# Optimization experiments

Hardware: AMD Instinct MI355X
Metric: run time of the kernel (lower is better)

The kernel has to match this reference:

```python
import jax, jax.numpy as jnp
import numpy as np

IN_FEATURES = 256
OUT_FEATURES = 128
ALPHA = 0.2  # LeakyReLU negative slope
NEG_INF = -9e15
N_NODES = 8192


def _xavier_uniform(key, shape, gain):
    fan_in, fan_out = shape[0], shape[1]
    limit = gain * np.sqrt(6.0 / (fan_in + fan_out))
    return jax.random.uniform(key, shape, jnp.float32, -limit, limit)


def setup_inputs() -> dict:
    key = jax.random.key(0)
    k_h, k_adj, k_W, k_a = jax.random.split(key, 4)
    h = jax.random.normal(k_h, (N_NODES, IN_FEATURES), dtype=jnp.float32)
    adj = jax.random.randint(k_adj, (N_NODES, N_NODES), 0, 2, dtype=jnp.int32)
    W = _xavier_uniform(k_W, (IN_FEATURES, OUT_FEATURES), gain=1.414)
    a = _xavier_uniform(k_a, (2 * OUT_FEATURES, 1), gain=1.414)
    return {"h": h, "adj": adj, "W": W, "a": a}


def reference(h, adj, W, a):
    # Wh: (N, F_out)
    Wh = h @ W
    # Decompose a = [a1; a2]; e_ij = leakyrelu(Wh_i . a1 + Wh_j . a2)
    # == the original concat([Wh_i, Wh_j]) @ a, without the O(N^2*2F) tensor.
    a1 = a[:OUT_FEATURES, 0]  # (F_out,)
    a2 = a[OUT_FEATURES:, 0]  # (F_out,)
    src = Wh @ a1  # (N,)
    dst = Wh @ a2  # (N,)
    e = jax.nn.leaky_relu(src[:, None] + dst[None, :], negative_slope=ALPHA)  # (N, N)
    attention = jnp.where(adj > 0, e, NEG_INF)
    attention = jax.nn.softmax(attention, axis=1)
    # dropout p=0.0 (eval) -> identity
    h_prime = attention @ Wh  # (N, F_out)
    return jax.nn.elu(h_prime)  # concat=True
```

## Files before the change

kernel.cpp:

```cpp
#include <hip/hip_runtime.h>

#define N_NODES 8192
#define IN_F    256
#define OUT_F   128
#define ALPHA_S 0.2f

typedef __attribute__((ext_vector_type(8))) short  short8;
typedef __attribute__((ext_vector_type(4))) short  short4v;
typedef __attribute__((ext_vector_type(4))) float  floatx4;
typedef __attribute__((ext_vector_type(4))) int    intx4;
typedef __attribute__((ext_vector_type(4))) float  fx4;

static __device__ __forceinline__ short f2bf(float f) {
    union { float f; unsigned int i; } u; u.f = f;
    unsigned int r = u.i + 0x7FFFu + ((u.i >> 16) & 1u);
    return (short)(r >> 16);
}

__global__ __launch_bounds__(512) void k_wh(
    const float* __restrict__ h,
    const float* __restrict__ W,
    const float* __restrict__ a,
    short* __restrict__ WhT,
    float* __restrict__ src,
    float* __restrict__ dst)
{
    __shared__ short Wt[OUT_F][IN_F + 8];
    __shared__ short htile[32][IN_F + 8];
    __shared__ float q1s[IN_F], q2s[IN_F];
    __shared__ short wh_t[OUT_F][40];

    const int t      = threadIdx.x;
    const int lane   = t & 63;
    const int wave   = t >> 6;
    const int r_base = blockIdx.x * 32;

#pragma unroll
    for (int rep = 0; rep < 4; ++rep) {
        const int idx = rep * 8192 + t * 16;
        const int k   = idx >> 7;
        const int f   = idx & 127;
        fx4 w0 = *(const fx4*)(W + idx);
        fx4 w1 = *(const fx4*)(W + idx + 4);
        fx4 w2 = *(const fx4*)(W + idx + 8);
        fx4 w3 = *(const fx4*)(W + idx + 12);
        fx4 a10 = *(const fx4*)(a + f);
        fx4 a11 = *(const fx4*)(a + f + 4);
        fx4 a12 = *(const fx4*)(a + f + 8);
        fx4 a13 = *(const fx4*)(a + f + 12);
        fx4 a20 = *(const fx4*)(a + OUT_F + f);
        fx4 a21 = *(const fx4*)(a + OUT_F + f + 4);
        fx4 a22 = *(const fx4*)(a + OUT_F + f + 8);
        fx4 a23 = *(const fx4*)(a + OUT_F + f + 12);
        float p1 = 0.f, p2 = 0.f;
#pragma unroll
        for (int e = 0; e < 4; ++e) {
            p1 = fmaf(w0[e], a10[e], p1); p2 = fmaf(w0[e], a20[e], p2);
            p1 = fmaf(w1[e], a11[e], p1); p2 = fmaf(w1[e], a21[e], p2);
            p1 = fmaf(w2[e], a12[e], p1); p2 = fmaf(w2[e], a22[e], p2);
            p1 = fmaf(w3[e], a13[e], p1); p2 = fmaf(w3[e], a23[e], p2);
        }
#pragma unroll
        for (int e = 0; e < 4; ++e) {
            Wt[f + e][k]      = f2bf(w0[e]);
            Wt[f + 4 + e][k]  = f2bf(w1[e]);
            Wt[f + 8 + e][k]  = f2bf(w2[e]);
            Wt[f + 12 + e][k] = f2bf(w3[e]);
        }
#pragma unroll
        for (int m = 1; m < 8; m <<= 1) {
            p1 += __shfl_xor(p1, m, 64);
            p2 += __shfl_xor(p2, m, 64);
        }
        if ((t & 7) == 0) { q1s[k] = p1; q2s[k] = p2; }
    }

    const int r0   = t >> 4;
    const int fgrp = t & 15;
    const int k0   = fgrp * 16;
    fx4 h0, h1, h2, h3;
    {
        const float* hp = h + (size_t)(r_base + r0) * IN_F + k0;
        h0 = *(const fx4*)hp; h1 = *(const fx4*)(hp + 4);
        h2 = *(const fx4*)(hp + 8); h3 = *(const fx4*)(hp + 12);
        short8 b0, b1;
#pragma unroll
        for (int e = 0; e < 4; ++e) {
            b0[e]     = f2bf(h0[e]); b0[4 + e] = f2bf(h1[e]);
            b1[e]     = f2bf(h2[e]); b1[4 + e] = f2bf(h3[e]);
        }
        *(short8*)&htile[r0][k0]     = b0;
        *(short8*)&htile[r0][k0 + 8] = b1;
    }
    __syncthreads();

    {
        float sp = 0.f, dp = 0.f;
#pragma unroll
        for (int e = 0; e < 4; ++e) {
            sp = fmaf(h0[e], q1s[k0 + e], sp);      dp = fmaf(h0[e], q2s[k0 + e], dp);
            sp = fmaf(h1[e], q1s[k0 + 4 + e], sp);  dp = fmaf(h1[e], q2s[k0 + 4 + e], dp);
            sp = fmaf(h2[e], q1s[k0 + 8 + e], sp);  dp = fmaf(h2[e], q2s[k0 + 8 + e], dp);
            sp = fmaf(h3[e], q1s[k0 + 12 + e], sp); dp = fmaf(h3[e], q2s[k0 + 12 + e], dp);
        }
#pragma unroll
        for (int m = 1; m < 16; m <<= 1) {
            sp += __shfl_xor(sp, m, 64);
            dp += __shfl_xor(dp, m, 64);
        }
        if (fgrp == 0) { src[r_base + r0] = sp; dst[r_base + r0] = dp; }
    }

    const int ln15 = lane & 15;
    const int q    = lane >> 4;
    const int f0   = wave * 16;
    floatx4 c0 = {0.f, 0.f, 0.f, 0.f};
    floatx4 c1 = {0.f, 0.f, 0.f, 0.f};
#pragma unroll
    for (int s = 0; s < 8; ++s) {
        short8 bf  = *(const short8*)&Wt[f0 + ln15][s * 32 + q * 8];
        short8 a0f = *(const short8*)&htile[ln15][s * 32 + q * 8];
        short8 a1f = *(const short8*)&htile[16 + ln15][s * 32 + q * 8];
        c0 = __builtin_amdgcn_mfma_f32_16x16x32_bf16(a0f, bf, c0, 0, 0, 0);
        c1 = __builtin_amdgcn_mfma_f32_16x16x32_bf16(a1f, bf, c1, 0, 0, 0);
    }
    {
        short4v p0, p1;
#pragma unroll
        for (int r = 0; r < 4; ++r) { p0[r] = f2bf(c0[r]); p1[r] = f2bf(c1[r]); }
        *(short4v*)&wh_t[f0 + ln15][q * 4]      = p0;
        *(short4v*)&wh_t[f0 + ln15][16 + q * 4] = p1;
    }
    __syncthreads();
    {
        const int f    = t >> 2;
        const int half = t & 3;
        *(short8*)(WhT + (size_t)f * N_NODES + r_base + half * 8) =
            *(const short8*)&wh_t[f][half * 8];
    }
}

#define JSPLIT 8
#define JCH    (N_NODES / JSPLIT)
#define SJ     64
#define NSTEP  (JCH / SJ)

__global__ __launch_bounds__(256, 4) void k_attn(
    const int*   __restrict__ adj,
    const short* __restrict__ WhT,
    const float* __restrict__ src,
    const float* __restrict__ dstv,
    float* __restrict__ numer_part,
    float* __restrict__ denom_part)
{
    const int t    = threadIdx.x;
    const int lane = t & 63;
    const int wave = t >> 6;
    const int rg   = blockIdx.x >> 3;
    const int jc   = blockIdx.x & 7;
    const int r0w  = rg * 64 + wave * 16;
    const int jb   = jc * JCH;

    const int ln15 = lane & 15;
    const int q    = lane >> 4;

    const float srow = src[r0w + ln15];
    const int*   ab = adj  + (size_t)(r0w + ln15) * N_NODES + jb + q * 8;
    const float* db = dstv + jb + q * 8;
    const short* bb = WhT + (size_t)ln15 * N_NODES + jb + q * 8;

    floatx4 acc[8];
#pragma unroll
    for (int ft = 0; ft < 8; ++ft) acc[ft] = (floatx4){0.f, 0.f, 0.f, 0.f};
    floatx4 dacc = {0.f, 0.f, 0.f, 0.f};
    short8 ones;
#pragma unroll
    for (int j = 0; j < 8; ++j) ones[j] = (short)0x3F80;

    intx4 m0 = *(const intx4*)(ab);
    intx4 m1 = *(const intx4*)(ab + 4);
    intx4 m2 = *(const intx4*)(ab + 32);
    intx4 m3 = *(const intx4*)(ab + 36);

    for (int s = 0; s < NSTEP; ++s) {
        const int off = s * SJ;
        intx4 c0 = m0, c1 = m1, c2 = m2, c3 = m3;
        if (s + 1 < NSTEP) {
            const int o2 = off + SJ;
            m0 = *(const intx4*)(ab + o2);
            m1 = *(const intx4*)(ab + o2 + 4);
            m2 = *(const intx4*)(ab + o2 + 32);
            m3 = *(const intx4*)(ab + o2 + 36);
        }
        fx4 d0 = *(const fx4*)(db + off);
        fx4 d1 = *(const fx4*)(db + off + 4);
        fx4 d2 = *(const fx4*)(db + off + 32);
        fx4 d3 = *(const fx4*)(db + off + 36);

        short8 A0, A1;
#pragma unroll
        for (int e = 0; e < 4; ++e) {
            float x, l;
            x = srow + d0[e]; l = fmaxf(x, ALPHA_S * x);
            A0[e]     = (c0[e] > 0) ? f2bf(__expf(l)) : (short)0;
            x = srow + d1[e]; l = fmaxf(x, ALPHA_S * x);
            A0[4 + e] = (c1[e] > 0) ? f2bf(__expf(l)) : (short)0;
            x = srow + d2[e]; l = fmaxf(x, ALPHA_S * x);
            A1[e]     = (c2[e] > 0) ? f2bf(__expf(l)) : (short)0;
            x = srow + d3[e]; l = fmaxf(x, ALPHA_S * x);
            A1[4 + e] = (c3[e] > 0) ? f2bf(__expf(l)) : (short)0;
        }

        dacc = __builtin_amdgcn_mfma_f32_16x16x32_bf16(A0, ones, dacc, 0, 0, 0);
        dacc = __builtin_amdgcn_mfma_f32_16x16x32_bf16(A1, ones, dacc, 0, 0, 0);

#pragma unroll
        for (int ft = 0; ft < 8; ++ft) {
            const short* bp = bb + (size_t)ft * 16 * N_NODES + off;
            short8 B0 = *(const short8*)bp;
            short8 B1 = *(const short8*)(bp + 32);
            acc[ft] = __builtin_amdgcn_mfma_f32_16x16x32_bf16(A0, B0, acc[ft], 0, 0, 0);
            acc[ft] = __builtin_amdgcn_mfma_f32_16x16x32_bf16(A1, B1, acc[ft], 0, 0, 0);
        }
    }

    float* np = numer_part + ((size_t)jc * N_NODES + r0w) * OUT_F;
#pragma unroll
    for (int ft = 0; ft < 8; ++ft)
#pragma unroll
        for (int r = 0; r < 4; ++r)
            np[(size_t)(q * 4 + r) * OUT_F + ft * 16 + ln15] = acc[ft][r];
    if (ln15 == 0) {
        float* dp = denom_part + (size_t)jc * N_NODES + r0w;
#pragma unroll
        for (int r = 0; r < 4; ++r) dp[q * 4 + r] = dacc[r];
    }
}

__global__ void k_final(const float* __restrict__ numer_part,
                        const float* __restrict__ denom_part,
                        float* __restrict__ out) {
    const int idx = blockIdx.x * 256 + threadIdx.x;
    const int row = idx >> 7;
    float v = 0.f, dn = 0.f;
#pragma unroll
    for (int jc = 0; jc < JSPLIT; ++jc) {
        v  += numer_part[(size_t)jc * N_NODES * OUT_F + idx];
        dn += denom_part[(size_t)jc * N_NODES + row];
    }
    v = (dn != 0.f) ? (v / dn) : 0.f;
    v = v > 0.f ? v : (__expf(v) - 1.f);
    out[idx] = v;
}

extern "C" void kernel_launch(void* const* d_in, const int* in_sizes, int n_in,
                              void* d_out, int out_size, void* d_ws, size_t ws_size,
                              hipStream_t stream) {
    const float* h   = (const float*)d_in[0];
    const int*   adj = (const int*)d_in[1];
    const float* W   = (const float*)d_in[2];
    const float* a   = (const float*)d_in[3];
    float* out = (float*)d_out;

    char*  ws         = (char*)d_ws;
    float* denom_part = (float*)ws;
    short* WhT        = (short*)(ws + (256 << 10));
    float* src        = (float*)(ws + (256 << 10) + (2 << 20));
    float* dst        = src + N_NODES;
    float* numer_part = (float*)(ws + (4 << 20));

    k_wh   <<<256, 512, 0, stream>>>(h, W, a, WhT, src, dst);
    k_attn <<<1024, 256, 0, stream>>>(adj, WhT, src, dst, numer_part, denom_part);
    k_final<<<4096, 256, 0, stream>>>(numer_part, denom_part, out);
}
```

Measured before the change: 470.7 us.

## Pre-swizzle Wh into MFMA fragment layout and double-buffer attention loads

k_wh now writes Wh in a blocked layout in which each wave's MFMA B-fragment is one contiguous 1 KB chunk, so k_attn reads it with coalesced loads instead of strided rows of a transposed matrix. k_attn stages the dst vector for its column chunk in shared memory and double-buffers both the adjacency and Wh fragment loads one step ahead in registers. The occupancy hint is lowered from 4 to 2 blocks per SIMD to make room for the larger register footprint, which costs latency hiding from concurrent waves.

```diff
diff --git a/kernel.cpp b/kernel.cpp
--- a/kernel.cpp
+++ b/kernel.cpp
@@ -21,7 +21,7 @@
     const float* __restrict__ h,
     const float* __restrict__ W,
     const float* __restrict__ a,
-    short* __restrict__ WhT,
+    short* __restrict__ WhB,
     float* __restrict__ src,
     float* __restrict__ dst)
 {
@@ -133,10 +133,12 @@
     }
     __syncthreads();
     {
-        const int f    = t >> 2;
-        const int half = t & 3;
-        *(short8*)(WhT + (size_t)f * N_NODES + r_base + half * 8) =
-            *(const short8*)&wh_t[f][half * 8];
+        const int ft2 = t >> 6;
+        const int l2  = t & 63;
+        const int n2  = l2 & 15;
+        const int q2  = l2 >> 4;
+        short8 v = *(const short8*)&wh_t[ft2 * 16 + n2][q2 * 8];
+        *(short8*)(WhB + (((size_t)blockIdx.x * 8 + ft2) * 64 + l2) * 8) = v;
     }
 }
 
@@ -145,14 +147,16 @@
 #define SJ     64
 #define NSTEP  (JCH / SJ)
 
-__global__ __launch_bounds__(256, 4) void k_attn(
+__global__ __launch_bounds__(256, 2) void k_attn(
     const int*   __restrict__ adj,
-    const short* __restrict__ WhT,
+    const short* __restrict__ WhB,
     const float* __restrict__ src,
     const float* __restrict__ dstv,
     float* __restrict__ numer_part,
     float* __restrict__ denom_part)
 {
+    __shared__ float dlds[JCH];
+
     const int t    = threadIdx.x;
     const int lane = t & 63;
     const int wave = t >> 6;
@@ -164,10 +168,12 @@
     const int ln15 = lane & 15;
     const int q    = lane >> 4;
 
+    *(fx4*)&dlds[t * 4] = *(const fx4*)(dstv + jb + t * 4);
+    __syncthreads();
+
     const float srow = src[r0w + ln15];
-    const int*   ab = adj  + (size_t)(r0w + ln15) * N_NODES + jb + q * 8;
-    const float* db = dstv + jb + q * 8;
-    const short* bb = WhT + (size_t)ln15 * N_NODES + jb + q * 8;
+    const int*   ab = adj + (size_t)(r0w + ln15) * N_NODES + jb + q * 8;
+    const short* wb = WhB + (size_t)(jc * 32) * 4096 + lane * 8;
 
     floatx4 acc[8];
 #pragma unroll
@@ -177,51 +183,57 @@
 #pragma unroll
     for (int j = 0; j < 8; ++j) ones[j] = (short)0x3F80;
 
-    intx4 m0 = *(const intx4*)(ab);
-    intx4 m1 = *(const intx4*)(ab + 4);
-    intx4 m2 = *(const intx4*)(ab + 32);
-    intx4 m3 = *(const intx4*)(ab + 36);
-
-    for (int s = 0; s < NSTEP; ++s) {
+    intx4  M0[4], M1[4];
+    short8 B0[16], B1[16];
+
+    auto loadstep = [&](int s, intx4* M, short8* B) {
         const int off = s * SJ;
-        intx4 c0 = m0, c1 = m1, c2 = m2, c3 = m3;
-        if (s + 1 < NSTEP) {
-            const int o2 = off + SJ;
-            m0 = *(const intx4*)(ab + o2);
-            m1 = *(const intx4*)(ab + o2 + 4);
-            m2 = *(const intx4*)(ab + o2 + 32);
-            m3 = *(const intx4*)(ab + o2 + 36);
-        }
-        fx4 d0 = *(const fx4*)(db + off);
-        fx4 d1 = *(const fx4*)(db + off + 4);
-        fx4 d2 = *(const fx4*)(db + off + 32);
-        fx4 d3 = *(const fx4*)(db + off + 36);
-
+        M[0] = *(const intx4*)(ab + off);
+        M[1] = *(const intx4*)(ab + off + 4);
+        M[2] = *(const intx4*)(ab + off + 32);
+        M[3] = *(const intx4*)(ab + off + 36);
+        const short* bs = wb + (size_t)(2 * s) * 4096;
+#pragma unroll
+        for (int ft = 0; ft < 8; ++ft) {
+            B[2 * ft]     = *(const short8*)(bs + ft * 512);
+            B[2 * ft + 1] = *(const short8*)(bs + 4096 + ft * 512);
+        }
+    };
+
+    auto compute = [&](int s, const intx4* M, const short8* B) {
+        const int off = s * SJ;
+        fx4 d0 = *(const fx4*)&dlds[off + q * 8];
+        fx4 d1 = *(const fx4*)&dlds[off + q * 8 + 4];
+        fx4 d2 = *(const fx4*)&dlds[off + 32 + q * 8];
+        fx4 d3 = *(const fx4*)&dlds[off + 32 + q * 8 + 4];
         short8 A0, A1;
 #pragma unroll
         for (int e = 0; e < 4; ++e) {
             float x, l;
             x = srow + d0[e]; l = fmaxf(x, ALPHA_S * x);
-            A0[e]     = (c0[e] > 0) ? f2bf(__expf(l)) : (short)0;
+            A0[e]     = (M[0][e] > 0) ? f2bf(__expf(l)) : (short)0;
             x = srow + d1[e]; l = fmaxf(x, ALPHA_S * x);
-            A0[4 + e] = (c1[e] > 0) ? f2bf(__expf(l)) : (short)0;
+            A0[4 + e] = (M[1][e] > 0) ? f2bf(__expf(l)) : (short)0;
             x = srow + d2[e]; l = fmaxf(x, ALPHA_S * x);
-            A1[e]     = (c2[e] > 0) ? f2bf(__expf(l)) : (short)0;
+            A1[e]     = (M[2][e] > 0) ? f2bf(__expf(l)) : (short)0;
             x = srow + d3[e]; l = fmaxf(x, ALPHA_S * x);
-            A1[4 + e] = (c3[e] > 0) ? f2bf(__expf(l)) : (short)0;
-        }
-
+            A1[4 + e] = (M[3][e] > 0) ? f2bf(__expf(l)) : (short)0;
+        }
         dacc = __builtin_amdgcn_mfma_f32_16x16x32_bf16(A0, ones, dacc, 0, 0, 0);
         dacc = __builtin_amdgcn_mfma_f32_16x16x32_bf16(A1, ones, dacc, 0, 0, 0);
-
 #pragma unroll
         for (int ft = 0; ft < 8; ++ft) {
-            const short* bp = bb + (size_t)ft * 16 * N_NODES + off;
-            short8 B0 = *(const short8*)bp;
-            short8 B1 = *(const short8*)(bp + 32);
-            acc[ft] = __builtin_amdgcn_mfma_f32_16x16x32_bf16(A0, B0, acc[ft], 0, 0, 0);
-            acc[ft] = __builtin_amdgcn_mfma_f32_16x16x32_bf16(A1, B1, acc[ft], 0, 0, 0);
-        }
+            acc[ft] = __builtin_amdgcn_mfma_f32_16x16x32_bf16(A0, B[2 * ft],     acc[ft], 0, 0, 0);
+            acc[ft] = __builtin_amdgcn_mfma_f32_16x16x32_bf16(A1, B[2 * ft + 1], acc[ft], 0, 0, 0);
+        }
+    };
+
+    loadstep(0, M0, B0);
+    for (int s = 0; s < NSTEP; s += 2) {
+        if (s + 1 < NSTEP) loadstep(s + 1, M1, B1);
+        compute(s, M0, B0);
+        if (s + 2 < NSTEP) loadstep(s + 2, M0, B0);
+        if (s + 1 < NSTEP) compute(s + 1, M1, B1);
     }
 
     float* np = numer_part + ((size_t)jc * N_NODES + r0w) * OUT_F;
@@ -264,12 +276,12 @@
 
     char*  ws         = (char*)d_ws;
     float* denom_part = (float*)ws;
-    short* WhT        = (short*)(ws + (256 << 10));
+    short* WhB        = (short*)(ws + (256 << 10));
     float* src        = (float*)(ws + (256 << 10) + (2 << 20));
     float* dst        = src + N_NODES;
     float* numer_part = (float*)(ws + (4 << 20));
 
-    k_wh   <<<256, 512, 0, stream>>>(h, W, a, WhT, src, dst);
-    k_attn <<<1024, 256, 0, stream>>>(adj, WhT, src, dst, numer_part, denom_part);
+    k_wh   <<<256, 512, 0, stream>>>(h, W, a, WhB, src, dst);
+    k_attn <<<1024, 256, 0, stream>>>(adj, WhB, src, dst, numer_part, denom_part);
     k_final<<<4096, 256, 0, stream>>>(numer_part, denom_part, out);
 }
```

Measured after the change: 413.4 us. -12.2%, faster.
